# Kernel optimization log

Hardware: AMD Instinct MI355X
Metric: run time of the kernel (lower is better)

Reference implementation:

```python
import jax, jax.numpy as jnp
import numpy as np

B, SEQ, ST, DIN, DK, DV = 2, 4096, 128, 1024, 64, 64
T = SEQ + 2 * ST  # 4352, divisible by 8 -> no pad branch in original


def _l2norm(t):
    # matches torch F.normalize(p=2, dim=-1, eps=1e-12)
    return t / jnp.maximum(jnp.linalg.norm(t, axis=-1, keepdims=True), 1e-12)


def setup_inputs() -> dict:
    key = jax.random.key(0)
    ks = jax.random.split(key, 9)
    x = jax.random.normal(ks[0], (B, T, DIN), dtype=jnp.float32)
    w = 0.02
    Wq = jax.random.normal(ks[1], (DK, DIN), dtype=jnp.float32) * w
    Wk = jax.random.normal(ks[2], (DK, DIN), dtype=jnp.float32) * w
    Wv = jax.random.normal(ks[3], (DV, DIN), dtype=jnp.float32) * w
    Wq_s = jax.random.normal(ks[4], (DK, DIN), dtype=jnp.float32) * w
    Wk_s = jax.random.normal(ks[5], (DK, DIN), dtype=jnp.float32) * w
    Wv_s = jax.random.normal(ks[6], (DV, DIN), dtype=jnp.float32) * w
    cope_emb = jax.random.normal(ks[7], (DK, T), dtype=jnp.float32)  # (1, dim_key, seq_len+2*state_len) squeezed
    scale = jnp.array([0.125], dtype=jnp.float32)  # learnable scaling_factor param
    return {"x": x, "Wq": Wq, "Wk": Wk, "Wv": Wv, "Wq_s": Wq_s,
            "Wk_s": Wk_s, "Wv_s": Wv_s, "cope_emb": cope_emb, "scale": scale}


def reference(x, Wq, Wk, Wv, Wq_s, Wk_s, Wv_s, cope_emb, scale):
    # extract_state: start-state, sequence, end-state
    xs, xm, xe = x[:, :ST], x[:, ST:ST + SEQ], x[:, ST + SEQ:]
    # project (Linear, no bias) then L2-normalize each token vector
    q = jnp.concatenate([_l2norm(xs @ Wq_s.T), _l2norm(xm @ Wq.T), _l2norm(xe @ Wq_s.T)], axis=1)
    k = jnp.concatenate([_l2norm(xs @ Wk_s.T), _l2norm(xm @ Wk.T), _l2norm(xe @ Wk_s.T)], axis=1)
    v = jnp.concatenate([_l2norm(xs @ Wv_s.T), _l2norm(xm @ Wv.T), _l2norm(xe @ Wv_s.T)], axis=1)

    # q@k^T is used both for CoPE gates and (scaled) attention scores
    logits = jnp.einsum('btd,bsd->bts', q, k)  # (B, T, T)

    # --- CoPE bias ---
    gates = jax.nn.sigmoid(logits)
    pos = jnp.cumsum(gates[:, :, ::-1], axis=-1)[:, :, ::-1]  # flip-cumsum-flip
    pos = jnp.minimum(pos, jnp.float32(T - 1))
    pos_floor = jnp.floor(pos)
    pos_ceil = jnp.ceil(pos)
    w = pos - pos_floor
    logits_int = jnp.einsum('btd,dl->btl', q, cope_emb)  # (B, T, T)
    lc = jnp.take_along_axis(logits_int, pos_ceil.astype(jnp.int32), axis=-1)
    lf = jnp.take_along_axis(logits_int, pos_floor.astype(jnp.int32), axis=-1)
    cope_bias = lc * w + lf * (1.0 - w)

    # --- causal + state-token mask: tril, with end-state rows blocked from start-state cols ---
    i = jnp.arange(T)
    mask = i[:, None] >= i[None, :]
    blocked = (i[:, None] >= SEQ + ST) & (i[None, :] < ST)
    mask = mask & (~blocked)
    attn_bias = jnp.where(mask, 0.0, -jnp.inf)[None, :, :]

    scores = logits * scale[0] + attn_bias + cope_bias
    att = jax.nn.softmax(scores, axis=-1) @ v  # (B, T, DV)
    return att
```

## Files before the change

kernel.cpp:

```cpp
#include <hip/hip_runtime.h>
#include <math.h>

#define B_ 2
#define SEQ_ 4096
#define ST_ 128
#define T_ 4352
#define DIN_ 1024
#define NW 16
#define LMAX 3328
#define LPAD 3336
#define NSLICE 272
#define NROW 8704

typedef _Float16 f16;
typedef __attribute__((ext_vector_type(8))) _Float16 f16x8;
typedef __attribute__((ext_vector_type(4))) float f32x4;

#define OB_WH  0
#define OB_WL  786432
#define OB_QH  1572864
#define OB_QL  2686976
#define OB_KH  3801088
#define OB_KL  4915200
#define OB_VT  6029312
#define OB_CPT 7143424
#define OB_SS  7569408
#define OB_XH  17039360
#define OB_XL  34865152
#define NEED_NEW 52690944ull

#define WT4_OFF 0
#define Q_OFF   393216
#define KT_OFF  950272
#define V_OFF   1507328

__device__ __forceinline__ int wuid() {
  return __builtin_amdgcn_readfirstlane((int)(threadIdx.x >> 6));
}

template<int CTRL, int RM>
__device__ __forceinline__ float dppadd(float x) {
  int y = __builtin_amdgcn_update_dpp(0, __float_as_int(x), CTRL, RM, 0xf, true);
  return x + __int_as_float(y);
}
__device__ __forceinline__ float wave_iscan(float x) {
  x = dppadd<0x111, 0xf>(x);
  x = dppadd<0x112, 0xf>(x);
  x = dppadd<0x114, 0xf>(x);
  x = dppadd<0x118, 0xf>(x);
  x = dppadd<0x142, 0xa>(x);
  x = dppadd<0x143, 0xc>(x);
  return x;
}
__device__ __forceinline__ float p16scan(float x) {
  x = dppadd<0x111, 0xf>(x);
  x = dppadd<0x112, 0xf>(x);
  x = dppadd<0x114, 0xf>(x);
  x = dppadd<0x118, 0xf>(x);
  return x;
}
__device__ __forceinline__ float swz15(float x) {
  return __int_as_float(__builtin_amdgcn_ds_swizzle(__float_as_int(x), 0x1F0));
}

__global__ __launch_bounds__(256) void wsplit_kernel(
    const float* __restrict__ Wq,  const float* __restrict__ Wk,
    const float* __restrict__ Wv,  const float* __restrict__ Wqs,
    const float* __restrict__ Wks, const float* __restrict__ Wvs,
    f16* __restrict__ wh, f16* __restrict__ wl) {
  const int m = blockIdx.y;
  const float* src = (m==0)?Wq:(m==1)?Wqs:(m==2)?Wk:(m==3)?Wks:(m==4)?Wv:Wvs;
  const int g0 = (int)blockIdx.x * 4096 + (int)threadIdx.x * 16;
  const float4* s4 = reinterpret_cast<const float4*>(src + g0);
  float4 v0 = s4[0], v1 = s4[1], v2 = s4[2], v3 = s4[3];
  f16x8 h0, h1, l0, l1;
  h0[0]=(f16)v0.x; h0[1]=(f16)v0.y; h0[2]=(f16)v0.z; h0[3]=(f16)v0.w;
  h0[4]=(f16)v1.x; h0[5]=(f16)v1.y; h0[6]=(f16)v1.z; h0[7]=(f16)v1.w;
  h1[0]=(f16)v2.x; h1[1]=(f16)v2.y; h1[2]=(f16)v2.z; h1[3]=(f16)v2.w;
  h1[4]=(f16)v3.x; h1[5]=(f16)v3.y; h1[6]=(f16)v3.z; h1[7]=(f16)v3.w;
  l0[0]=(f16)(v0.x-(float)h0[0]); l0[1]=(f16)(v0.y-(float)h0[1]);
  l0[2]=(f16)(v0.z-(float)h0[2]); l0[3]=(f16)(v0.w-(float)h0[3]);
  l0[4]=(f16)(v1.x-(float)h0[4]); l0[5]=(f16)(v1.y-(float)h0[5]);
  l0[6]=(f16)(v1.z-(float)h0[6]); l0[7]=(f16)(v1.w-(float)h0[7]);
  l1[0]=(f16)(v2.x-(float)h1[0]); l1[1]=(f16)(v2.y-(float)h1[1]);
  l1[2]=(f16)(v2.z-(float)h1[2]); l1[3]=(f16)(v2.w-(float)h1[3]);
  l1[4]=(f16)(v3.x-(float)h1[4]); l1[5]=(f16)(v3.y-(float)h1[5]);
  l1[6]=(f16)(v3.z-(float)h1[6]); l1[7]=(f16)(v3.w-(float)h1[7]);
  const size_t o = (size_t)m * 65536 + g0;
  *reinterpret_cast<f16x8*>(wh + o) = h0;
  *reinterpret_cast<f16x8*>(wh + o + 8) = h1;
  *reinterpret_cast<f16x8*>(wl + o) = l0;
  *reinterpret_cast<f16x8*>(wl + o + 8) = l1;
}

__global__ __launch_bounds__(256) void xsplit_kernel(
    const float* __restrict__ x, f16* __restrict__ xh, f16* __restrict__ xl) {
  const size_t g0 = ((size_t)blockIdx.x * 256 + threadIdx.x) * 16;
  const float4* s4 = reinterpret_cast<const float4*>(x + g0);
  float4 v0 = s4[0], v1 = s4[1], v2 = s4[2], v3 = s4[3];
  f16x8 h0, h1, l0, l1;
  h0[0]=(f16)v0.x; h0[1]=(f16)v0.y; h0[2]=(f16)v0.z; h0[3]=(f16)v0.w;
  h0[4]=(f16)v1.x; h0[5]=(f16)v1.y; h0[6]=(f16)v1.z; h0[7]=(f16)v1.w;
  h1[0]=(f16)v2.x; h1[1]=(f16)v2.y; h1[2]=(f16)v2.z; h1[3]=(f16)v2.w;
  h1[4]=(f16)v3.x; h1[5]=(f16)v3.y; h1[6]=(f16)v3.z; h1[7]=(f16)v3.w;
  l0[0]=(f16)(v0.x-(float)h0[0]); l0[1]=(f16)(v0.y-(float)h0[1]);
  l0[2]=(f16)(v0.z-(float)h0[2]); l0[3]=(f16)(v0.w-(float)h0[3]);
  l0[4]=(f16)(v1.x-(float)h0[4]); l0[5]=(f16)(v1.y-(float)h0[5]);
  l0[6]=(f16)(v1.z-(float)h0[6]); l0[7]=(f16)(v1.w-(float)h0[7]);
  l1[0]=(f16)(v2.x-(float)h1[0]); l1[1]=(f16)(v2.y-(float)h1[1]);
  l1[2]=(f16)(v2.z-(float)h1[2]); l1[3]=(f16)(v2.w-(float)h1[3]);
  l1[4]=(f16)(v3.x-(float)h1[4]); l1[5]=(f16)(v3.y-(float)h1[5]);
  l1[6]=(f16)(v3.z-(float)h1[6]); l1[7]=(f16)(v3.w-(float)h1[7]);
  *reinterpret_cast<f16x8*>(xh + g0) = h0;
  *reinterpret_cast<f16x8*>(xh + g0 + 8) = h1;
  *reinterpret_cast<f16x8*>(xl + g0) = l0;
  *reinterpret_cast<f16x8*>(xl + g0 + 8) = l1;
}

__global__ __launch_bounds__(256) void copet_kernel(
    const float* __restrict__ cope, f16* __restrict__ copeT) {
  __shared__ float t2[64][65];
  const int l0 = blockIdx.x << 6;
  const int tid = (int)threadIdx.x;
  #pragma unroll
  for (int p = 0; p < 16; ++p) {
    int d = (p << 2) + (tid >> 6), c = tid & 63;
    t2[d][c] = cope[(size_t)d * T_ + l0 + c];
  }
  __syncthreads();
  #pragma unroll
  for (int p = 0; p < 16; ++p) {
    int l = (p << 2) + (tid >> 6), d = tid & 63;
    copeT[(size_t)(l0 + l) * 64 + d] = (f16)t2[d][l];
  }
}

#define PM_MFMA(ACC, WHP, WLP) { \
  f16x8 bh_ = *reinterpret_cast<const f16x8*>((WHP) + (st << 5)); \
  f16x8 bl_ = *reinterpret_cast<const f16x8*>((WLP) + (st << 5)); \
  ACC = __builtin_amdgcn_mfma_f32_16x16x32_f16(xh_, bh_, ACC, 0, 0, 0); \
  ACC = __builtin_amdgcn_mfma_f32_16x16x32_f16(xl_, bh_, ACC, 0, 0, 0); \
  ACC = __builtin_amdgcn_mfma_f32_16x16x32_f16(xh_, bl_, ACC, 0, 0, 0); }

#define PM_RED(ACC, P) { \
  float s0_ = ACC[0]*ACC[0], s1_ = ACC[1]*ACC[1], s2_ = ACC[2]*ACC[2], s3_ = ACC[3]*ACC[3]; \
  s0_ += __shfl_xor(s0_, 1, 64); s1_ += __shfl_xor(s1_, 1, 64); \
  s2_ += __shfl_xor(s2_, 1, 64); s3_ += __shfl_xor(s3_, 1, 64); \
  s0_ += __shfl_xor(s0_, 2, 64); s1_ += __shfl_xor(s1_, 2, 64); \
  s2_ += __shfl_xor(s2_, 2, 64); s3_ += __shfl_xor(s3_, 2, 64); \
  s0_ += __shfl_xor(s0_, 4, 64); s1_ += __shfl_xor(s1_, 4, 64); \
  s2_ += __shfl_xor(s2_, 4, 64); s3_ += __shfl_xor(s3_, 4, 64); \
  s0_ += __shfl_xor(s0_, 8, 64); s1_ += __shfl_xor(s1_, 8, 64); \
  s2_ += __shfl_xor(s2_, 8, 64); s3_ += __shfl_xor(s3_, 8, 64); \
  if (qlo == 0) { \
    ssq[w][P][(qhi << 2) + 0] = s0_; ssq[w][P][(qhi << 2) + 1] = s1_; \
    ssq[w][P][(qhi << 2) + 2] = s2_; ssq[w][P][(qhi << 2) + 3] = s3_; } }

#define PM_QK1(ACC, P, HH, LL, RG) { \
  float tt_ = ssq[0][P][(qhi << 2) + RG] + ssq[1][P][(qhi << 2) + RG] \
            + ssq[2][P][(qhi << 2) + RG] + ssq[3][P][(qhi << 2) + RG]; \
  float rn_ = 1.f / fmaxf(sqrtf(tt_), 1e-12f); \
  float v_ = ACC[RG] * rn_; \
  f16 h_ = (f16)v_; \
  size_t ad_ = (size_t)(bt0 + (qhi << 2) + RG) * 64 + (w << 4) + qlo; \
  HH[ad_] = h_; LL[ad_] = (f16)(v_ - (float)h_); }

#define PM_V1(ACC, P, RG) { \
  float tt_ = ssq[0][P][(qhi << 2) + RG] + ssq[1][P][(qhi << 2) + RG] \
            + ssq[2][P][(qhi << 2) + RG] + ssq[3][P][(qhi << 2) + RG]; \
  float rn_ = 1.f / fmaxf(sqrtf(tt_), 1e-12f); \
  vt[(size_t)(b * 64 + (w << 4) + qlo) * T_ + t0 + (qhi << 2) + RG] = (f16)(ACC[RG] * rn_); }

__global__ __launch_bounds__(256, 4) void projM_kernel(
    const f16* __restrict__ xh, const f16* __restrict__ xl,
    const f16* __restrict__ wh, const f16* __restrict__ wl,
    f16* __restrict__ qh, f16* __restrict__ ql,
    f16* __restrict__ kh, f16* __restrict__ kl,
    f16* __restrict__ vt) {
  __shared__ float ssq[4][3][16];
  const int lane = (int)threadIdx.x & 63;
  const int w = wuid();
  const int qlo = lane & 15, qhi = lane >> 4;
  const int bt0 = (int)blockIdx.x << 4;
  const int b = bt0 / T_;
  const int t0 = bt0 - b * T_;
  const int spec = (t0 < ST_ || t0 >= ST_ + SEQ_) ? 1 : 0;

  const f16* xhr = xh + (size_t)(bt0 + qlo) * DIN_ + (qhi << 3);
  const f16* xlr = xl + (size_t)(bt0 + qlo) * DIN_ + (qhi << 3);
  const size_t wrow = (size_t)((w << 4) + qlo) * 1024 + (qhi << 3);
  const f16* wq  = wh + (size_t)(0 + spec) * 65536 + wrow;
  const f16* wqL = wl + (size_t)(0 + spec) * 65536 + wrow;
  const f16* wk  = wh + (size_t)(2 + spec) * 65536 + wrow;
  const f16* wkL = wl + (size_t)(2 + spec) * 65536 + wrow;
  const f16* wv  = wh + (size_t)(4 + spec) * 65536 + wrow;
  const f16* wvL = wl + (size_t)(4 + spec) * 65536 + wrow;

  f32x4 aq = {0.f,0.f,0.f,0.f}, ak = {0.f,0.f,0.f,0.f}, av = {0.f,0.f,0.f,0.f};

  #pragma unroll 4
  for (int st = 0; st < 32; ++st) {
    f16x8 xh_ = *reinterpret_cast<const f16x8*>(xhr + (st << 5));
    f16x8 xl_ = *reinterpret_cast<const f16x8*>(xlr + (st << 5));
    PM_MFMA(aq, wq, wqL)
    PM_MFMA(ak, wk, wkL)
    PM_MFMA(av, wv, wvL)
  }

  PM_RED(aq, 0) PM_RED(ak, 1) PM_RED(av, 2)
  __syncthreads();
  PM_QK1(aq, 0, qh, ql, 0) PM_QK1(aq, 0, qh, ql, 1)
  PM_QK1(aq, 0, qh, ql, 2) PM_QK1(aq, 0, qh, ql, 3)
  PM_QK1(ak, 1, kh, kl, 0) PM_QK1(ak, 1, kh, kl, 1)
  PM_QK1(ak, 1, kh, kl, 2) PM_QK1(ak, 1, kh, kl, 3)
  PM_V1(av, 2, 0) PM_V1(av, 2, 1) PM_V1(av, 2, 2) PM_V1(av, 2, 3)
}

__global__ __launch_bounds__(256) void gsum_kernel(
    const f16* __restrict__ qh, const f16* __restrict__ kh,
    float* __restrict__ ss) {
  const int lane = (int)threadIdx.x & 63;
  const int w = wuid();
  const int qlo = lane & 15, qhi = lane >> 4;
  const int chunk = blockIdx.x;
  const int bt0 = (int)blockIdx.y << 4;
  const int b = blockIdx.z;
  const int rowg0 = b * T_ + bt0;
  const size_t bT64 = (size_t)(b * T_) * 64;
  const f16* qrp = qh + (size_t)(rowg0 + qlo) * 64 + (qhi << 3);
  f16x8 aqh0 = *reinterpret_cast<const f16x8*>(qrp);
  f16x8 aqh1 = *reinterpret_cast<const f16x8*>(qrp + 32);
  #pragma unroll
  for (int nf = 0; nf < 8; ++nf) {
    const int colbase = (chunk << 9) + (w << 7) + (nf << 4);
    if (colbase < T_) {
      const int sg = colbase + qlo;
      const f16* krh_ = kh + bT64 + (size_t)sg * 64 + (qhi << 3);
      f16x8 bh0 = *reinterpret_cast<const f16x8*>(krh_);
      f16x8 bh1 = *reinterpret_cast<const f16x8*>(krh_ + 32);
      f32x4 a = {0.f, 0.f, 0.f, 0.f};
      a = __builtin_amdgcn_mfma_f32_16x16x32_f16(aqh0, bh0, a, 0, 0, 0);
      a = __builtin_amdgcn_mfma_f32_16x16x32_f16(aqh1, bh1, a, 0, 0, 0);
      float g0 = 1.f / (1.f + __expf(-a[0])); float s0 = p16scan(g0);
      float g1 = 1.f / (1.f + __expf(-a[1])); float s1 = p16scan(g1);
      float g2 = 1.f / (1.f + __expf(-a[2])); float s2 = p16scan(g2);
      float g3 = 1.f / (1.f + __expf(-a[3])); float s3 = p16scan(g3);
      if (qlo == 15) {
        const int sl = colbase >> 4;
        ss[(size_t)(rowg0 + (qhi << 2) + 0) * NSLICE + sl] = s0;
        ss[(size_t)(rowg0 + (qhi << 2) + 1) * NSLICE + sl] = s1;
        ss[(size_t)(rowg0 + (qhi << 2) + 2) * NSLICE + sl] = s2;
        ss[(size_t)(rowg0 + (qhi << 2) + 3) * NSLICE + sl] = s3;
      }
    }
  }
}

__global__ __launch_bounds__(1024) void sscan2_kernel(float* __restrict__ ss) {
  const int lane = (int)threadIdx.x & 63;
  const int w = wuid();
  const int row = (int)blockIdx.x * 16 + w;
  float* r = ss + (size_t)row * NSLICE;
  const int base = NSLICE - 1 - 5 * lane;
  double v0 = 0.0, v1 = 0.0, v2 = 0.0, v3 = 0.0, v4 = 0.0;
  double acc = 0.0;
  if (base - 0 >= 0) { acc += (double)r[base - 0]; } v0 = acc;
  if (base - 1 >= 0) { acc += (double)r[base - 1]; } v1 = acc;
  if (base - 2 >= 0) { acc += (double)r[base - 2]; } v2 = acc;
  if (base - 3 >= 0) { acc += (double)r[base - 3]; } v3 = acc;
  if (base - 4 >= 0) { acc += (double)r[base - 4]; } v4 = acc;
  double x = acc;
  #pragma unroll
  for (int off = 1; off < 64; off <<= 1) {
    double y = __shfl_up(x, off, 64);
    if (lane >= off) x += y;
  }
  const double offn = x - acc;
  if (base - 0 >= 0) r[base - 0] = (float)(v0 + offn);
  if (base - 1 >= 0) r[base - 1] = (float)(v1 + offn);
  if (base - 2 >= 0) r[base - 2] = (float)(v2 + offn);
  if (base - 3 >= 0) r[base - 3] = (float)(v3 + offn);
  if (base - 4 >= 0) r[base - 4] = (float)(v4 + offn);
}

#define QKD(SF, NF) { \
  int sg_ = swb + (NF << 4) + qlo; \
  int scl_ = sg_ < T_ ? sg_ : T_ - 1; \
  const f16* krh_ = kh + bT64 + (size_t)scl_ * 64 + (qhi << 3); \
  f16x8 bh0_ = *reinterpret_cast<const f16x8*>(krh_); \
  f16x8 bh1_ = *reinterpret_cast<const f16x8*>(krh_ + 32); \
  f32x4 a_ = {0.f, 0.f, 0.f, 0.f}; \
  a_ = __builtin_amdgcn_mfma_f32_16x16x32_f16(aqh0, bh0_, a_, 0, 0, 0); \
  a_ = __builtin_amdgcn_mfma_f32_16x16x32_f16(aqh1, bh1_, a_, 0, 0, 0); \
  SF = a_; }

#define PX(SF, NF, RG, SSV) { \
  int sg_ = swb + (NF << 4) + qlo; \
  float g_ = 1.f / (1.f + __expf(-SF[RG])); \
  float in_ = p16scan(g_); \
  float pos_ = SSV - in_ + g_; \
  pos_ = pos_ < 0.f ? 0.f : (pos_ > 3326.f ? 3326.f : pos_); \
  int idx_ = (int)pos_; \
  float wf_ = pos_ - (float)idx_; \
  const f16* lrow_ = liL + ((qhi << 2) + RG) * LPAD + idx_; \
  float lf_ = (float)lrow_[0], lc_ = (float)lrow_[1]; \
  float bias_ = fmaf(wf_, lc_ - lf_, lf_); \
  int tl_ = t0 + (qhi << 2) + RG; \
  bool valid_ = (sg_ <= tl_) && !((tl_ >= ST_ + SEQ_) && (sg_ < ST_)); \
  float p_ = valid_ ? __expf(fmaf(SF[RG], sc, bias_) - mrw[RG]) : 0.f; \
  lsum[RG] += p_; \
  pst[((qhi << 2) + RG) * 40 + (NF << 4) + qlo] = (f16)p_; }

#define PVF(OA, NF) { \
  int d_ = (NF << 4) + qlo; \
  const f16* vr_ = vt + (size_t)(b * 64 + d_) * T_; \
  f16x8 v0_ = *reinterpret_cast<const f16x8*>(vr_ + sv0); \
  OA = __builtin_amdgcn_mfma_f32_16x16x32_f16(pa0, v0_, OA, 0, 0, 0); }

#define OST(OA, NF) { \
  ob[w * 1024 + ((qhi << 2) + 0) * 64 + (NF << 4) + qlo] = OA[0]; \
  ob[w * 1024 + ((qhi << 2) + 1) * 64 + (NF << 4) + qlo] = OA[1]; \
  ob[w * 1024 + ((qhi << 2) + 2) * 64 + (NF << 4) + qlo] = OA[2]; \
  ob[w * 1024 + ((qhi << 2) + 3) * 64 + (NF << 4) + qlo] = OA[3]; }

__global__ __launch_bounds__(1024, 4) void attnD_kernel(
    const f16* __restrict__ qh, const f16* __restrict__ kh,
    const f16* __restrict__ vt, const f16* __restrict__ cpt,
    const float* __restrict__ ss,
    const float* __restrict__ scalep, float* __restrict__ out) {
  __shared__ __align__(16) f16 liL[16 * LPAD];
  __shared__ __align__(16) f16 pstage[NW * 16 * 40];
  __shared__ float totF[NW][16];
  __shared__ float rmxS[NW][16];

  const int tid = (int)threadIdx.x;
  const int lane = tid & 63;
  const int w = wuid();
  const int bt0 = ((int)(gridDim.x - 1 - blockIdx.x)) << 4;
  const int b = bt0 / T_;
  const int t0 = bt0 - b * T_;
  const float sc = scalep[0];
  const int qlo = lane & 15, qhi = lane >> 4;

  const f16* qrp = qh + (size_t)(bt0 + qlo) * 64 + (qhi << 3);
  f16x8 aqh0 = *reinterpret_cast<const f16x8*>(qrp);
  f16x8 aqh1 = *reinterpret_cast<const f16x8*>(qrp + 32);

  {
    f32x4 rm = {-1e30f, -1e30f, -1e30f, -1e30f};
    #pragma unroll 2
    for (int c = 0; c < 13; ++c) {
      const int lf = w * 208 + (c << 4);
      const f16* cr = cpt + (size_t)(lf + qlo) * 64 + (qhi << 3);
      f16x8 b0 = *reinterpret_cast<const f16x8*>(cr);
      f16x8 b1 = *reinterpret_cast<const f16x8*>(cr + 32);
      f32x4 a = {0.f, 0.f, 0.f, 0.f};
      a = __builtin_amdgcn_mfma_f32_16x16x32_f16(aqh0, b0, a, 0, 0, 0);
      a = __builtin_amdgcn_mfma_f32_16x16x32_f16(aqh1, b1, a, 0, 0, 0);
      f16 h0_ = (f16)a[0]; liL[((qhi << 2) + 0) * LPAD + lf + qlo] = h0_; rm[0] = fmaxf(rm[0], (float)h0_);
      f16 h1_ = (f16)a[1]; liL[((qhi << 2) + 1) * LPAD + lf + qlo] = h1_; rm[1] = fmaxf(rm[1], (float)h1_);
      f16 h2_ = (f16)a[2]; liL[((qhi << 2) + 2) * LPAD + lf + qlo] = h2_; rm[2] = fmaxf(rm[2], (float)h2_);
      f16 h3_ = (f16)a[3]; liL[((qhi << 2) + 3) * LPAD + lf + qlo] = h3_; rm[3] = fmaxf(rm[3], (float)h3_);
    }
    #pragma unroll
    for (int k = 1; k < 16; k <<= 1) {
      rm[0] = fmaxf(rm[0], __shfl_xor(rm[0], k, 64));
      rm[1] = fmaxf(rm[1], __shfl_xor(rm[1], k, 64));
      rm[2] = fmaxf(rm[2], __shfl_xor(rm[2], k, 64));
      rm[3] = fmaxf(rm[3], __shfl_xor(rm[3], k, 64));
    }
    if (qlo == 0) {
      rmxS[w][(qhi << 2) + 0] = rm[0];
      rmxS[w][(qhi << 2) + 1] = rm[1];
      rmxS[w][(qhi << 2) + 2] = rm[2];
      rmxS[w][(qhi << 2) + 3] = rm[3];
    }
  }
  __syncthreads();
  f32x4 mrw;
  #pragma unroll
  for (int reg = 0; reg < 4; ++reg) {
    float mm = rmxS[0][(qhi << 2) + reg];
    #pragma unroll
    for (int w2 = 1; w2 < NW; ++w2) mm = fmaxf(mm, rmxS[w2][(qhi << 2) + reg]);
    mrw[reg] = mm + fabsf(sc) + 2e-3f;
  }

  f16* pst = pstage + w * 640;
  const size_t bT64 = (size_t)(b * T_) * 64;
  const float* ssl = ss + (size_t)(bt0 + (qhi << 2)) * NSLICE;

  f32x4 o0 = {0.f,0.f,0.f,0.f}, o1 = {0.f,0.f,0.f,0.f};
  f32x4 o2 = {0.f,0.f,0.f,0.f}, o3 = {0.f,0.f,0.f,0.f};
  f32x4 lsum = {0.f,0.f,0.f,0.f};

  const int jtmax = (t0 + 15) >> 9;
  for (int jt = jtmax; jt >= 0; --jt) {
    const int swb = (jt << 9) + (w << 5);
    f32x4 sf0, sf1;
    QKD(sf0, 0) QKD(sf1, 1)
    const int sbr = swb >> 4;
    const int sb0 = sbr < (NSLICE - 1) ? sbr : (NSLICE - 1);
    const int sb1 = (sbr + 1) < (NSLICE - 1) ? (sbr + 1) : (NSLICE - 1);
    float sA0 = ssl[0 * NSLICE + sb0];
    float sA1 = ssl[1 * NSLICE + sb0];
    float sA2 = ssl[2 * NSLICE + sb0];
    float sA3 = ssl[3 * NSLICE + sb0];
    float sB0 = ssl[0 * NSLICE + sb1];
    float sB1 = ssl[1 * NSLICE + sb1];
    float sB2 = ssl[2 * NSLICE + sb1];
    float sB3 = ssl[3 * NSLICE + sb1];
    PX(sf0, 0, 0, sA0) PX(sf0, 0, 1, sA1) PX(sf0, 0, 2, sA2) PX(sf0, 0, 3, sA3)
    PX(sf1, 1, 0, sB0) PX(sf1, 1, 1, sB1) PX(sf1, 1, 2, sB2) PX(sf1, 1, 3, sB3)
    {
      const f16* pr = pst + qlo * 40;
      f16x8 pa0 = *reinterpret_cast<const f16x8*>(pr + (qhi << 3));
      int sv0 = swb + (qhi << 3);
      sv0 = sv0 < T_ - 8 ? sv0 : T_ - 8;
      PVF(o0, 0) PVF(o1, 1) PVF(o2, 2) PVF(o3, 3)
    }
  }

  #pragma unroll
  for (int k = 1; k < 16; k <<= 1) {
    lsum[0] += __shfl_xor(lsum[0], k, 64);
    lsum[1] += __shfl_xor(lsum[1], k, 64);
    lsum[2] += __shfl_xor(lsum[2], k, 64);
    lsum[3] += __shfl_xor(lsum[3], k, 64);
  }
  __syncthreads();
  if (qlo == 0) {
    totF[w][(qhi << 2) + 0] = lsum[0];
    totF[w][(qhi << 2) + 1] = lsum[1];
    totF[w][(qhi << 2) + 2] = lsum[2];
    totF[w][(qhi << 2) + 3] = lsum[3];
  }
  float* ob = reinterpret_cast<float*>(liL);
  OST(o0, 0) OST(o1, 1) OST(o2, 2) OST(o3, 3)
  __syncthreads();
  {
    const int r = tid >> 6, d = tid & 63;
    float L = 0.f, o = 0.f;
    #pragma unroll
    for (int w2 = 0; w2 < NW; ++w2) {
      L += totF[w2][r];
      o += ob[w2 * 1024 + tid];
    }
    out[(size_t)(bt0 + r) * 64 + d] = o / L;
  }
}

__global__ __launch_bounds__(256) void wtrans_kernel(
    const float* __restrict__ Wq,  const float* __restrict__ Wk,
    const float* __restrict__ Wv,  const float* __restrict__ Wqs,
    const float* __restrict__ Wks, const float* __restrict__ Wvs,
    float* __restrict__ ws) {
  const int m = blockIdx.y;
  const float* src = (m==0)?Wq:(m==1)?Wqs:(m==2)?Wk:(m==3)?Wks:(m==4)?Wv:Wvs;
  float* dst = ws + (size_t)m * (DIN_*64);
  const int bx = blockIdx.x;
  #pragma unroll
  for (int p = 0; p < 16; ++p) {
    int e = (int)threadIdx.x + (p << 8);
    int c = e & 3, o = (e >> 2) & 63;
    int i = (bx << 6) + (p << 2) + c;
    dst[(((bx << 4) + p) * 64 + o) * 4 + c] = src[o * DIN_ + i];
  }
}

__global__ __launch_bounds__(256) void proj_kernel(
    const float* __restrict__ x, float* __restrict__ ws) {
  __shared__ float tile[32][65];
  const int t0 = blockIdx.x << 5;
  const int b  = blockIdx.y;
  const int pj = blockIdx.z;
  const int spec = (t0 < ST_ || t0 >= ST_ + SEQ_) ? 1 : 0;
  const float4* W4 = reinterpret_cast<const float4*>(ws + WT4_OFF + (size_t)(pj*2 + spec) * (DIN_*64));
  const int lane = (int)threadIdx.x & 63;
  const int w = wuid();
  const float* xb = x + ((size_t)(b * T_ + t0 + (w << 3))) * DIN_;
  float acc[8] = {0.f,0.f,0.f,0.f,0.f,0.f,0.f,0.f};
  #pragma unroll 4
  for (int i4 = 0; i4 < 256; ++i4) {
    float4 wv = W4[(i4 << 6) + lane];
    #pragma unroll
    for (int r = 0; r < 8; ++r) {
      float4 xv = reinterpret_cast<const float4*>(xb + r * DIN_)[i4];
      acc[r] = fmaf(wv.x, xv.x, fmaf(wv.y, xv.y, fmaf(wv.z, xv.z, fmaf(wv.w, xv.w, acc[r]))));
    }
  }
  float outv[8];
  #pragma unroll
  for (int r = 0; r < 8; ++r) {
    float sq = acc[r] * acc[r];
    #pragma unroll
    for (int off = 32; off; off >>= 1) sq += __shfl_xor(sq, off, 64);
    float n = fmaxf(sqrtf(sq), 1e-12f);
    outv[r] = acc[r] / n;
  }
  const int trow = t0 + (w << 3);
  if (pj != 1) {
    float* dst = ws + (pj == 0 ? Q_OFF : V_OFF) + ((size_t)(b * T_ + trow)) * 64;
    #pragma unroll
    for (int r = 0; r < 8; ++r) dst[r * 64 + lane] = outv[r];
  } else {
    #pragma unroll
    for (int r = 0; r < 8; ++r) tile[(w << 3) + r][lane] = outv[r];
    __syncthreads();
    float* kt = ws + KT_OFF + (size_t)b * 16 * T_ * 4;
    #pragma unroll
    for (int p = 0; p < 8; ++p) {
      int e = (int)threadIdx.x + (p << 8);
      int c = e & 3, tt = (e >> 2) & 31, d4 = e >> 7;
      kt[((size_t)d4 * T_ + t0 + tt) * 4 + c] = tile[tt][(d4 << 2) + c];
    }
  }
}

__global__ __launch_bounds__(1024) void attn_kernel(
    const float* __restrict__ ws_c, const float* __restrict__ cope,
    const float* __restrict__ scalep, float* __restrict__ out) {
  __shared__ float li_s[8 * T_];
  __shared__ float pbuf[NW][8][32];
  __shared__ float totF[NW][8];
  __shared__ double suffD[NW][8];
  __shared__ double carryD[2][8];
  __shared__ float mlL[NW][8];
  __shared__ float wmax[NW][8];
  const int tid = (int)threadIdx.x;
  const int lane = tid & 63;
  const int w = wuid();
  const int t0 = ((int)(gridDim.x - 1 - blockIdx.x)) << 3;
  const int b  = blockIdx.y;
  const float* qrow = ws_c + Q_OFF + ((size_t)(b * T_ + t0)) * 64;
  const float* ktb  = ws_c + KT_OFF + (size_t)b * 16 * T_ * 4;
  const float* vb   = ws_c + V_OFF + ((size_t)b * T_) * 64;
  const float sc = scalep[0];
  if (tid < 8) carryD[0][tid] = 0.0;
  float lm[8];
  #pragma unroll
  for (int r = 0; r < 8; ++r) lm[r] = -INFINITY;
  for (int jt = 0; jt < 5; ++jt) {
    const int l = (jt << 10) + tid;
    if (l < T_) {
      float a[8] = {0,0,0,0,0,0,0,0};
      #pragma unroll 4
      for (int d4 = 0; d4 < 16; ++d4) {
        float c0 = cope[(d4 * 4 + 0) * T_ + l];
        float c1 = cope[(d4 * 4 + 1) * T_ + l];
        float c2 = cope[(d4 * 4 + 2) * T_ + l];
        float c3 = cope[(d4 * 4 + 3) * T_ + l];
        #pragma unroll
        for (int r = 0; r < 8; ++r) {
          float4 qq = *reinterpret_cast<const float4*>(qrow + r * 64 + (d4 << 2));
          a[r] = fmaf(c0, qq.x, fmaf(c1, qq.y, fmaf(c2, qq.z, fmaf(c3, qq.w, a[r]))));
        }
      }
      #pragma unroll
      for (int r = 0; r < 8; ++r) { li_s[r * T_ + l] = a[r]; lm[r] = fmaxf(lm[r], a[r]); }
    }
  }
  #pragma unroll
  for (int r = 0; r < 8; ++r) {
    #pragma unroll
    for (int off = 32; off; off >>= 1) lm[r] = fmaxf(lm[r], __shfl_xor(lm[r], off, 64));
  }
  if (lane == 0) {
    #pragma unroll
    for (int r = 0; r < 8; ++r) wmax[w][r] = lm[r];
  }
  __syncthreads();
  float mrow[8];
  #pragma unroll
  for (int r = 0; r < 8; ++r) {
    float mm = wmax[0][r];
    #pragma unroll
    for (int w2 = 1; w2 < NW; ++w2) mm = fmaxf(mm, wmax[w2][r]);
    mrow[r] = mm + fabsf(sc) + 1e-3f;
  }
  float acc[8]  = {0,0,0,0,0,0,0,0};
  float lsum[8] = {0,0,0,0,0,0,0,0};
  int par = 0;
  for (int jt = 4; jt >= 0; --jt) {
    const int s = (jt << 10) + tid;
    const bool sval = (s < T_);
    float lg[8] = {0,0,0,0,0,0,0,0};
    if (sval) {
      #pragma unroll 4
      for (int d4 = 0; d4 < 16; ++d4) {
        float4 kk = *reinterpret_cast<const float4*>(ktb + ((size_t)d4 * T_ + s) * 4);
        #pragma unroll
        for (int r = 0; r < 8; ++r) {
          float4 qq = *reinterpret_cast<const float4*>(qrow + r * 64 + (d4 << 2));
          lg[r] = fmaf(kk.x, qq.x, fmaf(kk.y, qq.y, fmaf(kk.z, qq.z, fmaf(kk.w, qq.w, lg[r]))));
        }
      }
    }
    float locsuf[8], gtot[8];
    #pragma unroll
    for (int r = 0; r < 8; ++r) {
      float g = sval ? 1.f / (1.f + __expf(-lg[r])) : 0.f;
      float xx = wave_iscan(g);
      float tt = __shfl(xx, 63, 64);
      locsuf[r] = tt - xx + g;
      gtot[r] = tt;
    }
    if (lane == 0) {
      #pragma unroll
      for (int r = 0; r < 8; ++r) totF[w][r] = gtot[r];
    }
    __syncthreads();
    if (tid < 128) {
      const int w2 = tid >> 3, r = tid & 7;
      float ssum = 0.f;
      for (int w3 = w2 + 1; w3 < NW; ++w3) ssum += totF[w3][r];
      suffD[w2][r] = carryD[par][r] + (double)ssum;
      if (w2 == 0) carryD[par ^ 1][r] = carryD[par][r] + (double)(ssum + totF[0][r]);
    }
    __syncthreads();
    par ^= 1;
    if ((jt << 10) > t0 + 7) continue;
    float p[8];
    #pragma unroll
    for (int r = 0; r < 8; ++r) {
      double posd = suffD[w][r] + (double)locsuf[r];
      if (posd > 4351.0) posd = 4351.0;
      int idx = (int)posd;
      float wf = (float)(posd - (double)idx);
      int idx2 = idx < 4351 ? idx + 1 : 4351;
      float lf = li_s[r * T_ + idx];
      float lc = li_s[r * T_ + idx2];
      float bias = fmaf(wf, lc - lf, lf);
      const int t = t0 + r;
      const bool valid = sval && (s <= t) && !((t >= ST_ + SEQ_) && (s < ST_));
      float score = valid ? fmaf(lg[r], sc, bias) : -INFINITY;
      p[r] = __expf(score - mrow[r]);
      lsum[r] += p[r];
    }
    const int sbase = (jt << 10) + (w << 6);
    if (sbase < T_) {
      #pragma unroll
      for (int pass = 0; pass < 2; ++pass) {
        if ((lane >> 5) == pass) {
          #pragma unroll
          for (int r = 0; r < 8; ++r) pbuf[w][r][lane & 31] = p[r];
        }
        const int s0 = sbase + (pass << 5);
        #pragma unroll 4
        for (int s4 = 0; s4 < 8; ++s4) {
          const int sb = s0 + (s4 << 2);
          float v0 = vb[(size_t)(sb + 0) * 64 + lane];
          float v1 = vb[(size_t)(sb + 1) * 64 + lane];
          float v2 = vb[(size_t)(sb + 2) * 64 + lane];
          float v3 = vb[(size_t)(sb + 3) * 64 + lane];
          #pragma unroll
          for (int r = 0; r < 8; ++r) {
            float4 pr = *reinterpret_cast<const float4*>(&pbuf[w][r][s4 << 2]);
            acc[r] = fmaf(pr.x, v0, fmaf(pr.y, v1, fmaf(pr.z, v2, fmaf(pr.w, v3, acc[r]))));
          }
        }
      }
    }
  }
  #pragma unroll
  for (int r = 0; r < 8; ++r) {
    #pragma unroll
    for (int off = 32; off; off >>= 1) lsum[r] += __shfl_xor(lsum[r], off, 64);
  }
  if (lane == 0) {
    #pragma unroll
    for (int r = 0; r < 8; ++r) mlL[w][r] = lsum[r];
  }
  float* pb = &pbuf[w][0][0];
  #pragma unroll
  for (int pass = 0; pass < 2; ++pass) {
    __syncthreads();
    #pragma unroll
    for (int rr = 0; rr < 4; ++rr) pb[rr * 64 + lane] = acc[pass * 4 + rr];
    __syncthreads();
    if (tid < 256) {
      const int rr = tid >> 6, d = tid & 63;
      const int r = pass * 4 + rr;
      float o = 0.f, L = 0.f;
      #pragma unroll
      for (int w2 = 0; w2 < NW; ++w2) {
        o += (&pbuf[w2][0][0])[rr * 64 + d];
        L += mlL[w2][r];
      }
      out[((size_t)(b * T_ + t0 + r)) * 64 + d] = o / L;
    }
  }
}

extern "C" void kernel_launch(void* const* d_in, const int* in_sizes, int n_in,
                              void* d_out, int out_size, void* d_ws, size_t ws_size,
                              hipStream_t stream) {
  const float* x    = (const float*)d_in[0];
  const float* Wq   = (const float*)d_in[1];
  const float* Wk   = (const float*)d_in[2];
  const float* Wv   = (const float*)d_in[3];
  const float* Wqs  = (const float*)d_in[4];
  const float* Wks  = (const float*)d_in[5];
  const float* Wvs  = (const float*)d_in[6];
  const float* cope = (const float*)d_in[7];
  const float* scl  = (const float*)d_in[8];
  float* outp = (float*)d_out;
  (void)in_sizes; (void)n_in; (void)out_size;

  if (ws_size >= NEED_NEW) {
    unsigned char* wb = (unsigned char*)d_ws;
    f16* whp = (f16*)(wb + OB_WH);
    f16* wlp = (f16*)(wb + OB_WL);
    f16* qh = (f16*)(wb + OB_QH);
    f16* ql = (f16*)(wb + OB_QL);
    f16* kh = (f16*)(wb + OB_KH);
    f16* kl = (f16*)(wb + OB_KL);
    f16* vt = (f16*)(wb + OB_VT);
    f16* cpt = (f16*)(wb + OB_CPT);
    float* ssp = (float*)(wb + OB_SS);
    f16* xhp = (f16*)(wb + OB_XH);
    f16* xlp = (f16*)(wb + OB_XL);
    hipLaunchKernelGGL(wsplit_kernel, dim3(16, 6), dim3(256), 0, stream,
                       Wq, Wk, Wv, Wqs, Wks, Wvs, whp, wlp);
    hipLaunchKernelGGL(xsplit_kernel, dim3(2176), dim3(256), 0, stream, x, xhp, xlp);
    hipLaunchKernelGGL(copet_kernel, dim3(52), dim3(256), 0, stream, cope, cpt);
    hipLaunchKernelGGL(projM_kernel, dim3(544), dim3(256), 0, stream,
                       xhp, xlp, whp, wlp, qh, ql, kh, kl, vt);
    hipLaunchKernelGGL(gsum_kernel, dim3(9, 272, 2), dim3(256), 0, stream,
                       qh, kh, ssp);
    hipLaunchKernelGGL(sscan2_kernel, dim3(544), dim3(1024), 0, stream, ssp);
    hipLaunchKernelGGL(attnD_kernel, dim3(544), dim3(1024), 0, stream,
                       qh, kh, vt, cpt, ssp, scl, outp);
  } else {
    float* ws = (float*)d_ws;
    hipLaunchKernelGGL(wtrans_kernel, dim3(16, 6), dim3(256), 0, stream,
                       Wq, Wk, Wv, Wqs, Wks, Wvs, ws);
    hipLaunchKernelGGL(proj_kernel, dim3(136, 2, 3), dim3(256), 0, stream, x, ws);
    hipLaunchKernelGGL(attn_kernel, dim3(544, 2), dim3(1024), 0, stream, ws, cope, scl, outp);
  }
}
```

Measured before the change: 261.0 us.

## Split projection K-loop across two wave groups and batch CoPE gathers

The projection kernel now runs 512 threads per block: two groups of four waves each handle half of the DIN reduction. The upper group writes its partial accumulators to shared memory, and the lower group adds them before normalising. This is meant to double the number of waves available to hide latency in the projection GEMM, at the cost of an extra shared-memory round trip and an additional barrier. In the attention kernel, the per-element CoPE work is split into two phases: all eight gathers from the logits_int table are issued first, and the bias, mask and exp math runs after. This lets those memory loads overlap, in exchange for higher register pressure.

```diff
diff --git a/kernel.cpp b/kernel.cpp
--- a/kernel.cpp
+++ b/kernel.cpp
@@ -153,8 +153,8 @@
   s0_ += __shfl_xor(s0_, 8, 64); s1_ += __shfl_xor(s1_, 8, 64); \
   s2_ += __shfl_xor(s2_, 8, 64); s3_ += __shfl_xor(s3_, 8, 64); \
   if (qlo == 0) { \
-    ssq[w][P][(qhi << 2) + 0] = s0_; ssq[w][P][(qhi << 2) + 1] = s1_; \
-    ssq[w][P][(qhi << 2) + 2] = s2_; ssq[w][P][(qhi << 2) + 3] = s3_; } }
+    ssq[wn][P][(qhi << 2) + 0] = s0_; ssq[wn][P][(qhi << 2) + 1] = s1_; \
+    ssq[wn][P][(qhi << 2) + 2] = s2_; ssq[wn][P][(qhi << 2) + 3] = s3_; } }
 
 #define PM_QK1(ACC, P, HH, LL, RG) { \
   float tt_ = ssq[0][P][(qhi << 2) + RG] + ssq[1][P][(qhi << 2) + RG] \
@@ -162,33 +162,37 @@
   float rn_ = 1.f / fmaxf(sqrtf(tt_), 1e-12f); \
   float v_ = ACC[RG] * rn_; \
   f16 h_ = (f16)v_; \
-  size_t ad_ = (size_t)(bt0 + (qhi << 2) + RG) * 64 + (w << 4) + qlo; \
+  size_t ad_ = (size_t)(bt0 + (qhi << 2) + RG) * 64 + (wn << 4) + qlo; \
   HH[ad_] = h_; LL[ad_] = (f16)(v_ - (float)h_); }
 
 #define PM_V1(ACC, P, RG) { \
   float tt_ = ssq[0][P][(qhi << 2) + RG] + ssq[1][P][(qhi << 2) + RG] \
             + ssq[2][P][(qhi << 2) + RG] + ssq[3][P][(qhi << 2) + RG]; \
   float rn_ = 1.f / fmaxf(sqrtf(tt_), 1e-12f); \
-  vt[(size_t)(b * 64 + (w << 4) + qlo) * T_ + t0 + (qhi << 2) + RG] = (f16)(ACC[RG] * rn_); }
-
-__global__ __launch_bounds__(256, 4) void projM_kernel(
+  vt[(size_t)(b * 64 + (wn << 4) + qlo) * T_ + t0 + (qhi << 2) + RG] = (f16)(ACC[RG] * rn_); }
+
+__global__ __launch_bounds__(512, 4) void projM_kernel(
     const f16* __restrict__ xh, const f16* __restrict__ xl,
     const f16* __restrict__ wh, const f16* __restrict__ wl,
     f16* __restrict__ qh, f16* __restrict__ ql,
     f16* __restrict__ kh, f16* __restrict__ kl,
     f16* __restrict__ vt) {
   __shared__ float ssq[4][3][16];
+  __shared__ float part[4][64][12];
   const int lane = (int)threadIdx.x & 63;
   const int w = wuid();
+  const int wn = w & 3;
+  const int kh2 = w >> 2;
   const int qlo = lane & 15, qhi = lane >> 4;
   const int bt0 = (int)blockIdx.x << 4;
   const int b = bt0 / T_;
   const int t0 = bt0 - b * T_;
   const int spec = (t0 < ST_ || t0 >= ST_ + SEQ_) ? 1 : 0;
 
-  const f16* xhr = xh + (size_t)(bt0 + qlo) * DIN_ + (qhi << 3);
-  const f16* xlr = xl + (size_t)(bt0 + qlo) * DIN_ + (qhi << 3);
-  const size_t wrow = (size_t)((w << 4) + qlo) * 1024 + (qhi << 3);
+  const int kof = kh2 << 9;
+  const f16* xhr = xh + (size_t)(bt0 + qlo) * DIN_ + kof + (qhi << 3);
+  const f16* xlr = xl + (size_t)(bt0 + qlo) * DIN_ + kof + (qhi << 3);
+  const size_t wrow = (size_t)((wn << 4) + qlo) * 1024 + kof + (qhi << 3);
   const f16* wq  = wh + (size_t)(0 + spec) * 65536 + wrow;
   const f16* wqL = wl + (size_t)(0 + spec) * 65536 + wrow;
   const f16* wk  = wh + (size_t)(2 + spec) * 65536 + wrow;
@@ -199,7 +203,7 @@
   f32x4 aq = {0.f,0.f,0.f,0.f}, ak = {0.f,0.f,0.f,0.f}, av = {0.f,0.f,0.f,0.f};
 
   #pragma unroll 4
-  for (int st = 0; st < 32; ++st) {
+  for (int st = 0; st < 16; ++st) {
     f16x8 xh_ = *reinterpret_cast<const f16x8*>(xhr + (st << 5));
     f16x8 xl_ = *reinterpret_cast<const f16x8*>(xlr + (st << 5));
     PM_MFMA(aq, wq, wqL)
@@ -207,13 +211,28 @@
     PM_MFMA(av, wv, wvL)
   }
 
-  PM_RED(aq, 0) PM_RED(ak, 1) PM_RED(av, 2)
+  if (w >= 4) {
+    float* p = &part[w - 4][lane][0];
+    p[0] = aq[0]; p[1] = aq[1]; p[2]  = aq[2]; p[3]  = aq[3];
+    p[4] = ak[0]; p[5] = ak[1]; p[6]  = ak[2]; p[7]  = ak[3];
+    p[8] = av[0]; p[9] = av[1]; p[10] = av[2]; p[11] = av[3];
+  }
   __syncthreads();
-  PM_QK1(aq, 0, qh, ql, 0) PM_QK1(aq, 0, qh, ql, 1)
-  PM_QK1(aq, 0, qh, ql, 2) PM_QK1(aq, 0, qh, ql, 3)
-  PM_QK1(ak, 1, kh, kl, 0) PM_QK1(ak, 1, kh, kl, 1)
-  PM_QK1(ak, 1, kh, kl, 2) PM_QK1(ak, 1, kh, kl, 3)
-  PM_V1(av, 2, 0) PM_V1(av, 2, 1) PM_V1(av, 2, 2) PM_V1(av, 2, 3)
+  if (w < 4) {
+    const float* p = &part[w][lane][0];
+    aq[0] += p[0]; aq[1] += p[1]; aq[2] += p[2];  aq[3] += p[3];
+    ak[0] += p[4]; ak[1] += p[5]; ak[2] += p[6];  ak[3] += p[7];
+    av[0] += p[8]; av[1] += p[9]; av[2] += p[10]; av[3] += p[11];
+    PM_RED(aq, 0) PM_RED(ak, 1) PM_RED(av, 2)
+  }
+  __syncthreads();
+  if (w < 4) {
+    PM_QK1(aq, 0, qh, ql, 0) PM_QK1(aq, 0, qh, ql, 1)
+    PM_QK1(aq, 0, qh, ql, 2) PM_QK1(aq, 0, qh, ql, 3)
+    PM_QK1(ak, 1, kh, kl, 0) PM_QK1(ak, 1, kh, kl, 1)
+    PM_QK1(ak, 1, kh, kl, 2) PM_QK1(ak, 1, kh, kl, 3)
+    PM_V1(av, 2, 0) PM_V1(av, 2, 1) PM_V1(av, 2, 2) PM_V1(av, 2, 3)
+  }
 }
 
 __global__ __launch_bounds__(256) void gsum_kernel(
@@ -294,17 +313,19 @@
   a_ = __builtin_amdgcn_mfma_f32_16x16x32_f16(aqh1, bh1_, a_, 0, 0, 0); \
   SF = a_; }
 
-#define PX(SF, NF, RG, SSV) { \
-  int sg_ = swb + (NF << 4) + qlo; \
+#define PXA(SF, RG, SSV, LF, LC, WF) { \
   float g_ = 1.f / (1.f + __expf(-SF[RG])); \
   float in_ = p16scan(g_); \
   float pos_ = SSV - in_ + g_; \
   pos_ = pos_ < 0.f ? 0.f : (pos_ > 3326.f ? 3326.f : pos_); \
   int idx_ = (int)pos_; \
-  float wf_ = pos_ - (float)idx_; \
+  WF = pos_ - (float)idx_; \
   const f16* lrow_ = liL + ((qhi << 2) + RG) * LPAD + idx_; \
-  float lf_ = (float)lrow_[0], lc_ = (float)lrow_[1]; \
-  float bias_ = fmaf(wf_, lc_ - lf_, lf_); \
+  LF = (float)lrow_[0]; LC = (float)lrow_[1]; }
+
+#define PXB(SF, NF, RG, LF, LC, WF) { \
+  int sg_ = swb + (NF << 4) + qlo; \
+  float bias_ = fmaf(WF, LC - LF, LF); \
   int tl_ = t0 + (qhi << 2) + RG; \
   bool valid_ = (sg_ <= tl_) && !((tl_ >= ST_ + SEQ_) && (sg_ < ST_)); \
   float p_ = valid_ ? __expf(fmaf(SF[RG], sc, bias_) - mrw[RG]) : 0.f; \
@@ -410,8 +431,16 @@
     float sB1 = ssl[1 * NSLICE + sb1];
     float sB2 = ssl[2 * NSLICE + sb1];
     float sB3 = ssl[3 * NSLICE + sb1];
-    PX(sf0, 0, 0, sA0) PX(sf0, 0, 1, sA1) PX(sf0, 0, 2, sA2) PX(sf0, 0, 3, sA3)
-    PX(sf1, 1, 0, sB0) PX(sf1, 1, 1, sB1) PX(sf1, 1, 2, sB2) PX(sf1, 1, 3, sB3)
+    float lf0, lc0, wf0, lf1, lc1, wf1, lf2, lc2, wf2, lf3, lc3, wf3;
+    float lf4, lc4, wf4, lf5, lc5, wf5, lf6, lc6, wf6, lf7, lc7, wf7;
+    PXA(sf0, 0, sA0, lf0, lc0, wf0) PXA(sf0, 1, sA1, lf1, lc1, wf1)
+    PXA(sf0, 2, sA2, lf2, lc2, wf2) PXA(sf0, 3, sA3, lf3, lc3, wf3)
+    PXA(sf1, 0, sB0, lf4, lc4, wf4) PXA(sf1, 1, sB1, lf5, lc5, wf5)
+    PXA(sf1, 2, sB2, lf6, lc6, wf6) PXA(sf1, 3, sB3, lf7, lc7, wf7)
+    PXB(sf0, 0, 0, lf0, lc0, wf0) PXB(sf0, 0, 1, lf1, lc1, wf1)
+    PXB(sf0, 0, 2, lf2, lc2, wf2) PXB(sf0, 0, 3, lf3, lc3, wf3)
+    PXB(sf1, 1, 0, lf4, lc4, wf4) PXB(sf1, 1, 1, lf5, lc5, wf5)
+    PXB(sf1, 1, 2, lf6, lc6, wf6) PXB(sf1, 1, 3, lf7, lc7, wf7)
     {
       const f16* pr = pst + qlo * 40;
       f16x8 pa0 = *reinterpret_cast<const f16x8*>(pr + (qhi << 3));
@@ -724,7 +753,7 @@
                        Wq, Wk, Wv, Wqs, Wks, Wvs, whp, wlp);
     hipLaunchKernelGGL(xsplit_kernel, dim3(2176), dim3(256), 0, stream, x, xhp, xlp);
     hipLaunchKernelGGL(copet_kernel, dim3(52), dim3(256), 0, stream, cope, cpt);
-    hipLaunchKernelGGL(projM_kernel, dim3(544), dim3(256), 0, stream,
+    hipLaunchKernelGGL(projM_kernel, dim3(544), dim3(512), 0, stream,
                        xhp, xlp, whp, wlp, qh, ql, kh, kl, vt);
     hipLaunchKernelGGL(gsum_kernel, dim3(9, 272, 2), dim3(256), 0, stream,
                        qh, kh, ssp);
```

Measured after the change: 255.3 us. -2.2%, faster.
